# Kernel tuning notes

Measured on AMD Instinct MI355X. Metric: run time of the kernel, lower is better.

The kernel has to match this reference:

```python
import jax, jax.numpy as jnp
import numpy as np

N_NODES = 100000
N_NEIGH = 10
DIM = 256
N_LAYERS = 3


def setup_inputs() -> dict:
    key = jax.random.key(0)
    ks = jax.random.split(key, 8)
    x = jax.random.normal(ks[0], (N_NODES, DIM), dtype=jnp.float32)
    adj = jax.random.randint(ks[1], (N_NODES, N_NEIGH), 0, N_NODES, dtype=jnp.int32)
    # per-layer SAGE weights: Linear(2*D -> D), stored as [2D, D] for x @ W
    scale = 0.05
    W0 = jax.random.normal(ks[2], (2 * DIM, DIM), dtype=jnp.float32) * scale
    W1 = jax.random.normal(ks[3], (2 * DIM, DIM), dtype=jnp.float32) * scale
    W2 = jax.random.normal(ks[4], (2 * DIM, DIM), dtype=jnp.float32) * scale
    b0 = jnp.zeros((DIM,), dtype=jnp.float32)
    b1 = jnp.zeros((DIM,), dtype=jnp.float32)
    b2 = jnp.zeros((DIM,), dtype=jnp.float32)
    return {"x": x, "adj": adj, "W0": W0, "b0": b0, "W1": W1, "b1": b1,
            "W2": W2, "b2": b2}


def reference(x, adj, W0, b0, W1, b1, W2, b2):
    """GraphSAGE: per layer, gather sampled neighbors [N,K,D], mean over K,
    concat with self embedding, linear [2D->D], ReLU on all but last layer."""
    layers = [(W0, b0), (W1, b1), (W2, b2)]
    h = x
    for i, (W, b) in enumerate(layers):
        neigh = jnp.mean(h[adj], axis=1)                 # [N, K, D] -> [N, D]
        h = jnp.concatenate([h, neigh], axis=1) @ W + b  # [N, 2D] @ [2D, D]
        if i < len(layers) - 1:
            h = jax.nn.relu(h)
    return h
```

## Files before the change

kernel.cpp:

```cpp
#include <hip/hip_runtime.h>
#include <stdint.h>

#define NN 100000
#define NK 10
#define D  256
#define D2 512
#define MT 32

typedef short bf16x8 __attribute__((ext_vector_type(8)));
typedef float f32x4  __attribute__((ext_vector_type(4)));

__device__ __forceinline__ uint16_t f2bf(float f) {
  uint32_t u = __float_as_uint(f);
  u += 0x7fffu + ((u >> 16) & 1u);
  return (uint16_t)(u >> 16);
}
__device__ __forceinline__ uint32_t pack2(float a, float b) {
  return (uint32_t)f2bf(a) | ((uint32_t)f2bf(b) << 16);
}

__global__ __launch_bounds__(256) void prep(
    const float* __restrict__ x, uint8_t* __restrict__ q8, float* __restrict__ qs,
    const float* __restrict__ W0, const float* __restrict__ W1,
    const float* __restrict__ W2, uint16_t* __restrict__ Wp0,
    uint16_t* __restrict__ Wp1, uint16_t* __restrict__ Wp2)
{
  const int bid = blockIdx.x;
  if (bid < 192) {
    const float* W;
    uint16_t* Wp;
    if (bid < 64)       { W = W0; Wp = Wp0; }
    else if (bid < 128) { W = W1; Wp = Wp1; }
    else                { W = W2; Wp = Wp2; }
    int idx   = ((bid & 63) << 8) + threadIdx.x;
    int lane  = idx & 63;
    int ntile = (idx >> 6) & 15;
    int kstep = idx >> 10;
    int n  = ntile * 16 + (lane & 15);
    int k0 = kstep * 32 + (lane >> 4) * 8;
    float v[8];
#pragma unroll
    for (int j = 0; j < 8; j++) v[j] = W[(size_t)(k0 + j) * D + n];
    uint4 o;
    o.x = pack2(v[0], v[1]);
    o.y = pack2(v[2], v[3]);
    o.z = pack2(v[4], v[5]);
    o.w = pack2(v[6], v[7]);
    ((uint4*)Wp)[idx] = o;
  } else {
    int node = (bid - 192) * 4 + (threadIdx.x >> 6);
    int lane = threadIdx.x & 63;
    const float4 v = *(const float4*)(x + (size_t)node * D + lane * 4);
    float m = fmaxf(fmaxf(fabsf(v.x), fabsf(v.y)), fmaxf(fabsf(v.z), fabsf(v.w)));
#pragma unroll
    for (int d = 1; d < 64; d <<= 1) m = fmaxf(m, __shfl_xor(m, d, 64));
    float inv = m > 1e-30f ? 127.0f / m : 0.0f;
    int q0 = (int)rintf(v.x * inv), q1 = (int)rintf(v.y * inv);
    int q2 = (int)rintf(v.z * inv), q3 = (int)rintf(v.w * inv);
    uint32_t p = (uint32_t)(q0 & 0xff) | ((uint32_t)(q1 & 0xff) << 8) |
                 ((uint32_t)(q2 & 0xff) << 16) | ((uint32_t)(q3 & 0xff) << 24);
    ((uint32_t*)(q8 + (size_t)node * D))[lane] = p;
    if (lane == 0) qs[node] = m * (1.0f / 127.0f);
  }
}

template <bool SELF_F32, bool QOUT>
__global__ __launch_bounds__(256, 4) void sage_layer(
    const void*     __restrict__ hin_v,
    const uint8_t*  __restrict__ qtab,
    const float*    __restrict__ qsc,
    const int*      __restrict__ adj,
    const uint16_t* __restrict__ Wp,
    const float*    __restrict__ bias,
    void*           __restrict__ hout_v,
    uint8_t*        __restrict__ q8out,
    float*          __restrict__ qsout)
{
  __shared__ uint4 lds4[MT * 64];
  const int t    = threadIdx.x;
  const int m0   = blockIdx.x * MT;
  const int half = t >> 5;
  const int l32  = t & 31;
  const int hb   = half & ~1;
  const int hsel = (half & 1) * 10;

  int av0, av1, av2, av3;
  {
    const int* ap = adj + (size_t)(m0 + hb) * NK;
    int o = (l32 < 20) ? l32 : 0;
    av0 = ap[o];
    av1 = ap[80 + o];
    av2 = ap[160 + o];
    av3 = ap[240 + o];
  }

  uint2 gA[NK], gB[NK];
  float sA[NK], sB[NK];

  auto issue = [&](int av, uint2 (&g)[NK], float (&s)[NK]) {
#pragma unroll
    for (int k = 0; k < NK; k++) {
      int nb = __shfl(av, hsel + k, 32);
      s[k] = qsc[nb];
      g[k] = *(const uint2*)(qtab + (size_t)nb * D + l32 * 8);
    }
  };
  auto consume = [&](const uint2 (&g)[NK], const float (&s)[NK], int i) {
    int r = i * 8 + half;
    float a0=0.f,a1=0.f,a2=0.f,a3=0.f,a4=0.f,a5=0.f,a6=0.f,a7=0.f;
#pragma unroll
    for (int k = 0; k < NK; k++) {
      float sk = s[k];
      uint2 v  = g[k];
      a0 += sk * (float)(int8_t)(v.x);
      a1 += sk * (float)(int8_t)(v.x >> 8);
      a2 += sk * (float)(int8_t)(v.x >> 16);
      a3 += sk * (float)(int8_t)(v.x >> 24);
      a4 += sk * (float)(int8_t)(v.y);
      a5 += sk * (float)(int8_t)(v.y >> 8);
      a6 += sk * (float)(int8_t)(v.y >> 16);
      a7 += sk * (float)(int8_t)(v.y >> 24);
    }
    const float sc = 1.0f / (float)NK;
    uint4 o;
    o.x = pack2(a0 * sc, a1 * sc);
    o.y = pack2(a2 * sc, a3 * sc);
    o.z = pack2(a4 * sc, a5 * sc);
    o.w = pack2(a6 * sc, a7 * sc);
    int c = 32 + l32;
    lds4[r * 64 + (c ^ (r & 15))] = o;
  };

  if constexpr (SELF_F32) {
#pragma unroll
    for (int i = 0; i < 4; i++) {
      int cidx = t + i * 256;
      int r = cidx >> 5, c = cidx & 31;
      const float4* p =
          (const float4*)((const float*)hin_v + (size_t)(m0 + r) * D + c * 8);
      float4 v0 = p[0], v1 = p[1];
      uint4 o;
      o.x = pack2(v0.x, v0.y); o.y = pack2(v0.z, v0.w);
      o.z = pack2(v1.x, v1.y); o.w = pack2(v1.z, v1.w);
      lds4[r * 64 + (c ^ (r & 15))] = o;
    }
    issue(av0, gA, sA);
    issue(av1, gB, sB);
  } else {
    uint4 p1[4];
#pragma unroll
    for (int i = 0; i < 4; i++) {
      int cidx = t + i * 256;
      int r = cidx >> 5, c = cidx & 31;
      p1[i] = *(const uint4*)((const uint16_t*)hin_v + (size_t)(m0 + r) * D + c * 8);
    }
    issue(av0, gA, sA);
    issue(av1, gB, sB);
#pragma unroll
    for (int i = 0; i < 4; i++) {
      int cidx = t + i * 256;
      int r = cidx >> 5, c = cidx & 31;
      lds4[r * 64 + (c ^ (r & 15))] = p1[i];
    }
  }

  consume(gA, sA, 0);
  issue(av2, gA, sA);
  consume(gB, sB, 1);
  issue(av3, gB, sB);
  consume(gA, sA, 2);
  consume(gB, sB, 3);

  __syncthreads();

  const int w    = t >> 6;
  const int l    = t & 63;
  const int quad = l >> 4;
  const int l16  = l & 15;

  f32x4 acc[2][4];
#pragma unroll
  for (int mt = 0; mt < 2; mt++)
#pragma unroll
    for (int nt = 0; nt < 4; nt++)
      acc[mt][nt] = (f32x4){0.f, 0.f, 0.f, 0.f};

  const uint4* wp4 = (const uint4*)Wp;

#pragma unroll 2
  for (int ks = 0; ks < 16; ks++) {
    bf16x8 af[2], bfr[4];
#pragma unroll
    for (int mt = 0; mt < 2; mt++) {
      int row = mt * 16 + l16;
      int c   = ks * 4 + quad;
      af[mt] = *((const bf16x8*)&lds4[row * 64 + (c ^ (row & 15))]);
    }
#pragma unroll
    for (int nt = 0; nt < 4; nt++) {
      bfr[nt] = *((const bf16x8*)&wp4[(ks * 16 + (w * 4 + nt)) * 64 + l]);
    }
#pragma unroll
    for (int mt = 0; mt < 2; mt++)
#pragma unroll
      for (int nt = 0; nt < 4; nt++)
        acc[mt][nt] = __builtin_amdgcn_mfma_f32_16x16x32_bf16(
            af[mt], bfr[nt], acc[mt][nt], 0, 0, 0);
  }

  float lmax[2][4];
#pragma unroll
  for (int mt = 0; mt < 2; mt++)
#pragma unroll
    for (int i = 0; i < 4; i++) lmax[mt][i] = 0.0f;

#pragma unroll
  for (int mt = 0; mt < 2; mt++)
#pragma unroll
    for (int nt = 0; nt < 4; nt++)
#pragma unroll
      for (int i = 0; i < 4; i++) {
        int col = w * 64 + nt * 16 + l16;
        float v = acc[mt][nt][i] + bias[col];
        if (QOUT) v = fmaxf(v, 0.0f);
        acc[mt][nt][i] = v;
        if (QOUT) lmax[mt][i] = fmaxf(lmax[mt][i], v);
      }

  float inv[2][4];
  if (QOUT) {
#pragma unroll
    for (int d = 1; d < 16; d <<= 1)
#pragma unroll
      for (int mt = 0; mt < 2; mt++)
#pragma unroll
        for (int i = 0; i < 4; i++)
          lmax[mt][i] = fmaxf(lmax[mt][i], __shfl_xor(lmax[mt][i], d, 64));
    __syncthreads();
    float* rmax = (float*)lds4;
    if (l16 == 0) {
#pragma unroll
      for (int mt = 0; mt < 2; mt++)
#pragma unroll
        for (int i = 0; i < 4; i++)
          rmax[(mt * 16 + quad * 4 + i) * 4 + w] = lmax[mt][i];
    }
    __syncthreads();
#pragma unroll
    for (int mt = 0; mt < 2; mt++)
#pragma unroll
      for (int i = 0; i < 4; i++) {
        int row = mt * 16 + quad * 4 + i;
        float m = fmaxf(fmaxf(rmax[row * 4 + 0], rmax[row * 4 + 1]),
                        fmaxf(rmax[row * 4 + 2], rmax[row * 4 + 3]));
        inv[mt][i] = m > 1e-30f ? 127.0f / m : 0.0f;
        if (w == 0 && l16 == 0) qsout[m0 + row] = m * (1.0f / 127.0f);
      }
  }

#pragma unroll
  for (int mt = 0; mt < 2; mt++)
#pragma unroll
    for (int i = 0; i < 4; i++) {
      int rr = m0 + mt * 16 + quad * 4 + i;
#pragma unroll
      for (int nt = 0; nt < 4; nt++) {
        int col = w * 64 + nt * 16 + l16;
        float v = acc[mt][nt][i];
        if (QOUT) {
          ((uint16_t*)hout_v)[(size_t)rr * D + col] = f2bf(v);
          int q = (int)rintf(v * inv[mt][i]);
          q8out[(size_t)rr * D + col] = (uint8_t)(q & 0xff);
        } else {
          ((float*)hout_v)[(size_t)rr * D + col] = v;
        }
      }
    }
}

extern "C" void kernel_launch(void* const* d_in, const int* in_sizes, int n_in,
                              void* d_out, int out_size, void* d_ws, size_t ws_size,
                              hipStream_t stream) {
  const float* x   = (const float*)d_in[0];
  const int*   adj = (const int*)d_in[1];
  const float* W0  = (const float*)d_in[2];
  const float* b0  = (const float*)d_in[3];
  const float* W1  = (const float*)d_in[4];
  const float* b1  = (const float*)d_in[5];
  const float* W2  = (const float*)d_in[6];
  const float* b2  = (const float*)d_in[7];
  float* out = (float*)d_out;

  uint8_t*  dob = (uint8_t*)d_out;
  uint16_t* hA  = (uint16_t*)dob;
  uint8_t*  hA8 = dob + 51200000;
  uint8_t*  x8  = dob + 76800000;

  uint16_t* ws  = (uint16_t*)d_ws;
  uint16_t* Wp0 = ws;
  uint16_t* Wp1 = Wp0 + D2 * D;
  uint16_t* Wp2 = Wp1 + D2 * D;
  uint16_t* hB  = Wp2 + D2 * D;
  uint8_t*  hB8 = (uint8_t*)(hB + (size_t)NN * D);
  float*    xs  = (float*)(hB8 + (size_t)NN * D);
  float*    hAs = xs + NN;
  float*    hBs = hAs + NN;

  prep<<<192 + NN / 4, 256, 0, stream>>>(x, x8, xs, W0, W1, W2, Wp0, Wp1, Wp2);

  const int grid = NN / MT;
  sage_layer<true,  true ><<<grid, 256, 0, stream>>>(x,  x8,  xs,  adj, Wp0, b0, hA,  hA8, hAs);
  sage_layer<false, true ><<<grid, 256, 0, stream>>>(hA, hA8, hAs, adj, Wp1, b1, hB,  hB8, hBs);
  sage_layer<false, false><<<grid, 256, 0, stream>>>(hB, hB8, hBs, adj, Wp2, b2, out, nullptr, nullptr);
}
```

Measured before the change: 427.4 us.

## Stream neighbor gathers directly into LDS with per-wave async pipeline

```diff
diff --git a/kernel.cpp b/kernel.cpp
--- a/kernel.cpp
+++ b/kernel.cpp
@@ -17,6 +17,12 @@
 }
 __device__ __forceinline__ uint32_t pack2(float a, float b) {
   return (uint32_t)f2bf(a) | ((uint32_t)f2bf(b) << 16);
+}
+
+__device__ __forceinline__ void gload_lds4(const void* g, void* lds) {
+  __builtin_amdgcn_global_load_lds(
+      (const __attribute__((address_space(1))) uint32_t*)g,
+      (__attribute__((address_space(3))) uint32_t*)lds, 4, 0, 0);
 }
 
 __global__ __launch_bounds__(256) void prep(
@@ -65,7 +71,7 @@
 }
 
 template <bool SELF_F32, bool QOUT>
-__global__ __launch_bounds__(256, 4) void sage_layer(
+__global__ __launch_bounds__(256, 3) void sage_layer(
     const void*     __restrict__ hin_v,
     const uint8_t*  __restrict__ qtab,
     const float*    __restrict__ qsc,
@@ -76,105 +82,103 @@
     uint8_t*        __restrict__ q8out,
     float*          __restrict__ qsout)
 {
-  __shared__ uint4 lds4[MT * 64];
-  const int t    = threadIdx.x;
-  const int m0   = blockIdx.x * MT;
-  const int half = t >> 5;
-  const int l32  = t & 31;
-  const int hb   = half & ~1;
-  const int hsel = (half & 1) * 10;
-
-  int av0, av1, av2, av3;
-  {
-    const int* ap = adj + (size_t)(m0 + hb) * NK;
-    int o = (l32 < 20) ? l32 : 0;
-    av0 = ap[o];
-    av1 = ap[80 + o];
-    av2 = ap[160 + o];
-    av3 = ap[240 + o];
-  }
-
-  uint2 gA[NK], gB[NK];
-  float sA[NK], sB[NK];
-
-  auto issue = [&](int av, uint2 (&g)[NK], float (&s)[NK]) {
-#pragma unroll
-    for (int k = 0; k < NK; k++) {
-      int nb = __shfl(av, hsel + k, 32);
-      s[k] = qsc[nb];
-      g[k] = *(const uint2*)(qtab + (size_t)nb * D + l32 * 8);
-    }
-  };
-  auto consume = [&](const uint2 (&g)[NK], const float (&s)[NK], int i) {
-    int r = i * 8 + half;
-    float a0=0.f,a1=0.f,a2=0.f,a3=0.f,a4=0.f,a5=0.f,a6=0.f,a7=0.f;
-#pragma unroll
-    for (int k = 0; k < NK; k++) {
-      float sk = s[k];
-      uint2 v  = g[k];
-      a0 += sk * (float)(int8_t)(v.x);
-      a1 += sk * (float)(int8_t)(v.x >> 8);
-      a2 += sk * (float)(int8_t)(v.x >> 16);
-      a3 += sk * (float)(int8_t)(v.x >> 24);
-      a4 += sk * (float)(int8_t)(v.y);
-      a5 += sk * (float)(int8_t)(v.y >> 8);
-      a6 += sk * (float)(int8_t)(v.y >> 16);
-      a7 += sk * (float)(int8_t)(v.y >> 24);
-    }
-    const float sc = 1.0f / (float)NK;
-    uint4 o;
-    o.x = pack2(a0 * sc, a1 * sc);
-    o.y = pack2(a2 * sc, a3 * sc);
-    o.z = pack2(a4 * sc, a5 * sc);
-    o.w = pack2(a6 * sc, a7 * sc);
-    int c = 32 + l32;
-    lds4[r * 64 + (c ^ (r & 15))] = o;
-  };
-
-  if constexpr (SELF_F32) {
-#pragma unroll
-    for (int i = 0; i < 4; i++) {
-      int cidx = t + i * 256;
-      int r = cidx >> 5, c = cidx & 31;
+  __shared__ uint4    lds4[MT * 64];
+  __shared__ uint32_t stg[4 * 2 * NK * 64];
+
+  const int t  = threadIdx.x;
+  const int m0 = blockIdx.x * MT;
+  const int w  = t >> 6;
+  const int l  = t & 63;
+
+  const int* ap = adj + (size_t)(m0 + 8 * w) * NK;
+  int av0 = ap[l];
+  int av1 = ap[64 + (l & 15)];
+  __builtin_amdgcn_sched_barrier(0);
+
+  float4 sv[4][2];
+  uint4  sb[4];
+#pragma unroll
+  for (int i = 0; i < 4; i++) {
+    int cidx = t + i * 256;
+    int r = cidx >> 5, c = cidx & 31;
+    if constexpr (SELF_F32) {
       const float4* p =
           (const float4*)((const float*)hin_v + (size_t)(m0 + r) * D + c * 8);
-      float4 v0 = p[0], v1 = p[1];
-      uint4 o;
-      o.x = pack2(v0.x, v0.y); o.y = pack2(v0.z, v0.w);
-      o.z = pack2(v1.x, v1.y); o.w = pack2(v1.z, v1.w);
-      lds4[r * 64 + (c ^ (r & 15))] = o;
-    }
-    issue(av0, gA, sA);
-    issue(av1, gB, sB);
-  } else {
-    uint4 p1[4];
-#pragma unroll
-    for (int i = 0; i < 4; i++) {
-      int cidx = t + i * 256;
-      int r = cidx >> 5, c = cidx & 31;
-      p1[i] = *(const uint4*)((const uint16_t*)hin_v + (size_t)(m0 + r) * D + c * 8);
-    }
-    issue(av0, gA, sA);
-    issue(av1, gB, sB);
-#pragma unroll
-    for (int i = 0; i < 4; i++) {
-      int cidx = t + i * 256;
-      int r = cidx >> 5, c = cidx & 31;
-      lds4[r * 64 + (c ^ (r & 15))] = p1[i];
-    }
-  }
-
-  consume(gA, sA, 0);
-  issue(av2, gA, sA);
-  consume(gB, sB, 1);
-  issue(av3, gB, sB);
-  consume(gA, sA, 2);
-  consume(gB, sB, 3);
+      sv[i][0] = p[0];
+      sv[i][1] = p[1];
+    } else {
+      sb[i] = *(const uint4*)((const uint16_t*)hin_v + (size_t)(m0 + r) * D + c * 8);
+    }
+  }
+  __builtin_amdgcn_sched_barrier(0);
+
+  float sp0 = qsc[av0];
+  float sp1 = qsc[av1];
+  __builtin_amdgcn_sched_barrier(0);
+
+  auto issue_row = [&](int r) {
+#pragma unroll
+    for (int k = 0; k < NK; k++) {
+      const int j = r * NK + k;
+      int nb = (j < 64) ? __shfl(av0, j, 64) : __shfl(av1, j - 64, 64);
+      gload_lds4(qtab + (size_t)nb * D + l * 4,
+                 &stg[(((w << 1) | (r & 1)) * NK + k) * 64]);
+    }
+  };
+
+  issue_row(0);
+  issue_row(1);
+  __builtin_amdgcn_sched_barrier(0);
+
+#pragma unroll
+  for (int i = 0; i < 4; i++) {
+    int cidx = t + i * 256;
+    int r = cidx >> 5, c = cidx & 31;
+    uint4 o;
+    if constexpr (SELF_F32) {
+      o.x = pack2(sv[i][0].x, sv[i][0].y);
+      o.y = pack2(sv[i][0].z, sv[i][0].w);
+      o.z = pack2(sv[i][1].x, sv[i][1].y);
+      o.w = pack2(sv[i][1].z, sv[i][1].w);
+    } else {
+      o = sb[i];
+    }
+    lds4[r * 64 + (c ^ (r & 15))] = o;
+  }
+  __builtin_amdgcn_sched_barrier(0);
+
+  const float scK = 1.0f / (float)NK;
+#pragma unroll
+  for (int r = 0; r < 8; r++) {
+    if (r < 7) asm volatile("s_waitcnt vmcnt(10)" ::: "memory");
+    else       asm volatile("s_waitcnt vmcnt(0)"  ::: "memory");
+    __builtin_amdgcn_sched_barrier(0);
+
+    float c0 = 0.f, c1 = 0.f, c2 = 0.f, c3 = 0.f;
+#pragma unroll
+    for (int k = 0; k < NK; k++) {
+      const int j = r * NK + k;
+      float s = (j < 64) ? __shfl(sp0, j, 64) : __shfl(sp1, j - 64, 64);
+      uint32_t v = stg[(((w << 1) | (r & 1)) * NK + k) * 64 + l];
+      c0 += s * (float)(int8_t)(v);
+      c1 += s * (float)(int8_t)(v >> 8);
+      c2 += s * (float)(int8_t)(v >> 16);
+      c3 += s * (float)(int8_t)(v >> 24);
+    }
+    uint2 o;
+    o.x = pack2(c0 * scK, c1 * scK);
+    o.y = pack2(c2 * scK, c3 * scK);
+    const int r8 = 8 * w + r;
+    const int cc = 32 + (l >> 1);
+    *(uint2*)((uint8_t*)lds4 +
+              ((r8 * 64 + (cc ^ (r8 & 15))) * 16 + (l & 1) * 8)) = o;
+    __builtin_amdgcn_sched_barrier(0);
+    if (r < 6) issue_row(r + 2);
+    __builtin_amdgcn_sched_barrier(0);
+  }
 
   __syncthreads();
 
-  const int w    = t >> 6;
-  const int l    = t & 63;
   const int quad = l >> 4;
   const int l16  = l & 15;
 
```

Measured after the change: 492.2 us. 15.1% more time.

## Hand-schedule gather loads with inline asm and explicit vmcnt waits

Applied to the files above, without the earlier changes.

```diff
diff --git a/kernel.cpp b/kernel.cpp
--- a/kernel.cpp
+++ b/kernel.cpp
@@ -9,6 +9,9 @@
 
 typedef short bf16x8 __attribute__((ext_vector_type(8)));
 typedef float f32x4  __attribute__((ext_vector_type(4)));
+typedef unsigned int vu2a __attribute__((ext_vector_type(2)));
+typedef unsigned int vu4a __attribute__((ext_vector_type(4)));
+typedef float        vf4  __attribute__((ext_vector_type(4)));
 
 __device__ __forceinline__ uint16_t f2bf(float f) {
   uint32_t u = __float_as_uint(f);
@@ -18,6 +21,25 @@
 __device__ __forceinline__ uint32_t pack2(float a, float b) {
   return (uint32_t)f2bf(a) | ((uint32_t)f2bf(b) << 16);
 }
+
+__device__ __forceinline__ void gl_f32(float &d, uint64_t a) {
+  asm volatile("global_load_dword %0, %1, off" : "=v"(d) : "v"(a));
+}
+__device__ __forceinline__ void gl_b64(vu2a &d, uint64_t a) {
+  asm volatile("global_load_dwordx2 %0, %1, off" : "=v"(d) : "v"(a));
+}
+__device__ __forceinline__ void gl_b128(vu4a &d, uint64_t a) {
+  asm volatile("global_load_dwordx4 %0, %1, off" : "=v"(d) : "v"(a));
+}
+#define VMWAIT(N)                                            \
+  do {                                                       \
+    asm volatile("s_waitcnt vmcnt(" #N ")" ::: "memory");    \
+    __builtin_amdgcn_sched_barrier(0);                       \
+  } while (0)
+__device__ __forceinline__ void vsync_i(int &x)    { asm volatile("" : "+v"(x)); }
+__device__ __forceinline__ void vsync_f(float &x)  { asm volatile("" : "+v"(x)); }
+__device__ __forceinline__ void vsync_u2(vu2a &x)  { asm volatile("" : "+v"(x)); }
+__device__ __forceinline__ void vsync_u4(vu4a &x)  { asm volatile("" : "+v"(x)); }
 
 __global__ __launch_bounds__(256) void prep(
     const float* __restrict__ x, uint8_t* __restrict__ q8, float* __restrict__ qs,
@@ -50,7 +72,7 @@
   } else {
     int node = (bid - 192) * 4 + (threadIdx.x >> 6);
     int lane = threadIdx.x & 63;
-    const float4 v = *(const float4*)(x + (size_t)node * D + lane * 4);
+    const vf4 v = *(const vf4*)(x + (size_t)node * D + lane * 4);
     float m = fmaxf(fmaxf(fabsf(v.x), fabsf(v.y)), fmaxf(fabsf(v.z), fabsf(v.w)));
 #pragma unroll
     for (int d = 1; d < 64; d <<= 1) m = fmaxf(m, __shfl_xor(m, d, 64));
@@ -86,32 +108,52 @@
 
   int av0, av1, av2, av3;
   {
-    const int* ap = adj + (size_t)(m0 + hb) * NK;
     int o = (l32 < 20) ? l32 : 0;
-    av0 = ap[o];
-    av1 = ap[80 + o];
-    av2 = ap[160 + o];
-    av3 = ap[240 + o];
-  }
-
-  uint2 gA[NK], gB[NK];
+    uint64_t aa = (uint64_t)(adj + (size_t)(m0 + hb) * NK + o);
+    asm volatile("global_load_dword %0, %1, off"            : "=v"(av0) : "v"(aa));
+    asm volatile("global_load_dword %0, %1, off offset:320" : "=v"(av1) : "v"(aa));
+    asm volatile("global_load_dword %0, %1, off offset:640" : "=v"(av2) : "v"(aa));
+    asm volatile("global_load_dword %0, %1, off offset:960" : "=v"(av3) : "v"(aa));
+  }
+
+  vu4a p1[4];
+  vu4a pf[8];
+#pragma unroll
+  for (int i = 0; i < 4; i++) {
+    int cidx = t + i * 256;
+    int r = cidx >> 5, c = cidx & 31;
+    if constexpr (SELF_F32) {
+      uint64_t a = (uint64_t)((const float*)hin_v + (size_t)(m0 + r) * D + c * 8);
+      gl_b128(pf[2 * i], a);
+      gl_b128(pf[2 * i + 1], a + 16);
+    } else {
+      uint64_t a = (uint64_t)((const uint16_t*)hin_v + (size_t)(m0 + r) * D + c * 8);
+      gl_b128(p1[i], a);
+    }
+  }
+
+  vu2a gA[NK], gB[NK];
   float sA[NK], sB[NK];
 
-  auto issue = [&](int av, uint2 (&g)[NK], float (&s)[NK]) {
+  auto issue = [&](int av, vu2a (&g)[NK], float (&s)[NK]) {
 #pragma unroll
     for (int k = 0; k < NK; k++) {
       int nb = __shfl(av, hsel + k, 32);
-      s[k] = qsc[nb];
-      g[k] = *(const uint2*)(qtab + (size_t)nb * D + l32 * 8);
+      gl_f32(s[k], (uint64_t)(qsc + nb));
+      gl_b64(g[k], (uint64_t)(qtab + (size_t)nb * D + l32 * 8));
     }
   };
-  auto consume = [&](const uint2 (&g)[NK], const float (&s)[NK], int i) {
+  auto sync_buf = [&](vu2a (&g)[NK], float (&s)[NK]) {
+#pragma unroll
+    for (int k = 0; k < NK; k++) { vsync_u2(g[k]); vsync_f(s[k]); }
+  };
+  auto consume = [&](const vu2a (&g)[NK], const float (&s)[NK], int i) {
     int r = i * 8 + half;
     float a0=0.f,a1=0.f,a2=0.f,a3=0.f,a4=0.f,a5=0.f,a6=0.f,a7=0.f;
 #pragma unroll
     for (int k = 0; k < NK; k++) {
       float sk = s[k];
-      uint2 v  = g[k];
+      vu2a v  = g[k];
       a0 += sk * (float)(int8_t)(v.x);
       a1 += sk * (float)(int8_t)(v.x >> 8);
       a2 += sk * (float)(int8_t)(v.x >> 16);
@@ -131,44 +173,59 @@
     lds4[r * 64 + (c ^ (r & 15))] = o;
   };
 
-  if constexpr (SELF_F32) {
+  auto self_to_lds = [&]() {
 #pragma unroll
     for (int i = 0; i < 4; i++) {
       int cidx = t + i * 256;
       int r = cidx >> 5, c = cidx & 31;
-      const float4* p =
-          (const float4*)((const float*)hin_v + (size_t)(m0 + r) * D + c * 8);
-      float4 v0 = p[0], v1 = p[1];
       uint4 o;
-      o.x = pack2(v0.x, v0.y); o.y = pack2(v0.z, v0.w);
-      o.z = pack2(v1.x, v1.y); o.w = pack2(v1.z, v1.w);
+      if constexpr (SELF_F32) {
+        vu4a v0 = pf[2 * i], v1 = pf[2 * i + 1];
+        o.x = pack2(__uint_as_float(v0.x), __uint_as_float(v0.y));
+        o.y = pack2(__uint_as_float(v0.z), __uint_as_float(v0.w));
+        o.z = pack2(__uint_as_float(v1.x), __uint_as_float(v1.y));
+        o.w = pack2(__uint_as_float(v1.z), __uint_as_float(v1.w));
+      } else {
+        vu4a v = p1[i];
+        o.x = v.x; o.y = v.y; o.z = v.z; o.w = v.w;
+      }
       lds4[r * 64 + (c ^ (r & 15))] = o;
     }
+  };
+
+  if constexpr (SELF_F32) {
+    VMWAIT(8);
+    vsync_i(av0); vsync_i(av1); vsync_i(av2); vsync_i(av3);
     issue(av0, gA, sA);
+    VMWAIT(20);
+#pragma unroll
+    for (int i = 0; i < 8; i++) vsync_u4(pf[i]);
+    self_to_lds();
     issue(av1, gB, sB);
+    VMWAIT(20);
   } else {
-    uint4 p1[4];
-#pragma unroll
-    for (int i = 0; i < 4; i++) {
-      int cidx = t + i * 256;
-      int r = cidx >> 5, c = cidx & 31;
-      p1[i] = *(const uint4*)((const uint16_t*)hin_v + (size_t)(m0 + r) * D + c * 8);
-    }
+    VMWAIT(4);
+    vsync_i(av0); vsync_i(av1); vsync_i(av2); vsync_i(av3);
     issue(av0, gA, sA);
+    VMWAIT(20);
+#pragma unroll
+    for (int i = 0; i < 4; i++) vsync_u4(p1[i]);
+    self_to_lds();
     issue(av1, gB, sB);
-#pragma unroll
-    for (int i = 0; i < 4; i++) {
-      int cidx = t + i * 256;
-      int r = cidx >> 5, c = cidx & 31;
-      lds4[r * 64 + (c ^ (r & 15))] = p1[i];
-    }
-  }
-
+    VMWAIT(20);
+  }
+  sync_buf(gA, sA);
   consume(gA, sA, 0);
   issue(av2, gA, sA);
+  VMWAIT(20);
+  sync_buf(gB, sB);
   consume(gB, sB, 1);
   issue(av3, gB, sB);
+  VMWAIT(20);
+  sync_buf(gA, sA);
   consume(gA, sA, 2);
+  VMWAIT(0);
+  sync_buf(gB, sB);
   consume(gB, sB, 3);
 
   __syncthreads();
```

Result: no change. 424.3 us (-0.7%).

## Halve node tile to 16 rows per block and double occupancy target

Applied to the files above, without the earlier changes.

```diff
diff --git a/kernel.cpp b/kernel.cpp
--- a/kernel.cpp
+++ b/kernel.cpp
@@ -5,7 +5,7 @@
 #define NK 10
 #define D  256
 #define D2 512
-#define MT 32
+#define MT 16
 
 typedef short bf16x8 __attribute__((ext_vector_type(8)));
 typedef float f32x4  __attribute__((ext_vector_type(4)));
@@ -65,7 +65,7 @@
 }
 
 template <bool SELF_F32, bool QOUT>
-__global__ __launch_bounds__(256, 4) void sage_layer(
+__global__ __launch_bounds__(256, 8) void sage_layer(
     const void*     __restrict__ hin_v,
     const uint8_t*  __restrict__ qtab,
     const float*    __restrict__ qsc,
@@ -84,14 +84,12 @@
   const int hb   = half & ~1;
   const int hsel = (half & 1) * 10;
 
-  int av0, av1, av2, av3;
+  int av0, av1;
   {
     const int* ap = adj + (size_t)(m0 + hb) * NK;
     int o = (l32 < 20) ? l32 : 0;
     av0 = ap[o];
     av1 = ap[80 + o];
-    av2 = ap[160 + o];
-    av3 = ap[240 + o];
   }
 
   uint2 gA[NK], gB[NK];
@@ -133,7 +131,7 @@
 
   if constexpr (SELF_F32) {
 #pragma unroll
-    for (int i = 0; i < 4; i++) {
+    for (int i = 0; i < 2; i++) {
       int cidx = t + i * 256;
       int r = cidx >> 5, c = cidx & 31;
       const float4* p =
@@ -147,9 +145,9 @@
     issue(av0, gA, sA);
     issue(av1, gB, sB);
   } else {
-    uint4 p1[4];
-#pragma unroll
-    for (int i = 0; i < 4; i++) {
+    uint4 p1[2];
+#pragma unroll
+    for (int i = 0; i < 2; i++) {
       int cidx = t + i * 256;
       int r = cidx >> 5, c = cidx & 31;
       p1[i] = *(const uint4*)((const uint16_t*)hin_v + (size_t)(m0 + r) * D + c * 8);
@@ -157,7 +155,7 @@
     issue(av0, gA, sA);
     issue(av1, gB, sB);
 #pragma unroll
-    for (int i = 0; i < 4; i++) {
+    for (int i = 0; i < 2; i++) {
       int cidx = t + i * 256;
       int r = cidx >> 5, c = cidx & 31;
       lds4[r * 64 + (c ^ (r & 15))] = p1[i];
@@ -165,11 +163,7 @@
   }
 
   consume(gA, sA, 0);
-  issue(av2, gA, sA);
   consume(gB, sB, 1);
-  issue(av3, gB, sB);
-  consume(gA, sA, 2);
-  consume(gB, sB, 3);
 
   __syncthreads();
 
@@ -178,104 +172,86 @@
   const int quad = l >> 4;
   const int l16  = l & 15;
 
-  f32x4 acc[2][4];
-#pragma unroll
-  for (int mt = 0; mt < 2; mt++)
-#pragma unroll
-    for (int nt = 0; nt < 4; nt++)
-      acc[mt][nt] = (f32x4){0.f, 0.f, 0.f, 0.f};
+  f32x4 acc[4];
+#pragma unroll
+  for (int nt = 0; nt < 4; nt++)
+    acc[nt] = (f32x4){0.f, 0.f, 0.f, 0.f};
 
   const uint4* wp4 = (const uint4*)Wp;
 
 #pragma unroll 2
   for (int ks = 0; ks < 16; ks++) {
-    bf16x8 af[2], bfr[4];
-#pragma unroll
-    for (int mt = 0; mt < 2; mt++) {
-      int row = mt * 16 + l16;
+    bf16x8 af, bfr[4];
+    {
+      int row = l16;
       int c   = ks * 4 + quad;
-      af[mt] = *((const bf16x8*)&lds4[row * 64 + (c ^ (row & 15))]);
+      af = *((const bf16x8*)&lds4[row * 64 + (c ^ (row & 15))]);
     }
 #pragma unroll
     for (int nt = 0; nt < 4; nt++) {
       bfr[nt] = *((const bf16x8*)&wp4[(ks * 16 + (w * 4 + nt)) * 64 + l]);
     }
 #pragma unroll
-    for (int mt = 0; mt < 2; mt++)
-#pragma unroll
-      for (int nt = 0; nt < 4; nt++)
-        acc[mt][nt] = __builtin_amdgcn_mfma_f32_16x16x32_bf16(
-            af[mt], bfr[nt], acc[mt][nt], 0, 0, 0);
-  }
-
-  float lmax[2][4];
-#pragma unroll
-  for (int mt = 0; mt < 2; mt++)
-#pragma unroll
-    for (int i = 0; i < 4; i++) lmax[mt][i] = 0.0f;
-
-#pragma unroll
-  for (int mt = 0; mt < 2; mt++)
-#pragma unroll
     for (int nt = 0; nt < 4; nt++)
-#pragma unroll
-      for (int i = 0; i < 4; i++) {
-        int col = w * 64 + nt * 16 + l16;
-        float v = acc[mt][nt][i] + bias[col];
-        if (QOUT) v = fmaxf(v, 0.0f);
-        acc[mt][nt][i] = v;
-        if (QOUT) lmax[mt][i] = fmaxf(lmax[mt][i], v);
-      }
-
-  float inv[2][4];
+      acc[nt] = __builtin_amdgcn_mfma_f32_16x16x32_bf16(af, bfr[nt], acc[nt], 0, 0, 0);
+  }
+
+  float lmax[4];
+#pragma unroll
+  for (int i = 0; i < 4; i++) lmax[i] = 0.0f;
+
+#pragma unroll
+  for (int nt = 0; nt < 4; nt++)
+#pragma unroll
+    for (int i = 0; i < 4; i++) {
+      int col = w * 64 + nt * 16 + l16;
+      float v = acc[nt][i] + bias[col];
+      if (QOUT) v = fmaxf(v, 0.0f);
+      acc[nt][i] = v;
+      if (QOUT) lmax[i] = fmaxf(lmax[i], v);
+    }
+
+  float inv[4];
   if (QOUT) {
 #pragma unroll
     for (int d = 1; d < 16; d <<= 1)
 #pragma unroll
-      for (int mt = 0; mt < 2; mt++)
-#pragma unroll
-        for (int i = 0; i < 4; i++)
-          lmax[mt][i] = fmaxf(lmax[mt][i], __shfl_xor(lmax[mt][i], d, 64));
+      for (int i = 0; i < 4; i++)
+        lmax[i] = fmaxf(lmax[i], __shfl_xor(lmax[i], d, 64));
     __syncthreads();
     float* rmax = (float*)lds4;
     if (l16 == 0) {
 #pragma unroll
-      for (int mt = 0; mt < 2; mt++)
-#pragma unroll
-        for (int i = 0; i < 4; i++)
-          rmax[(mt * 16 + quad * 4 + i) * 4 + w] = lmax[mt][i];
+      for (int i = 0; i < 4; i++)
+        rmax[(quad * 4 + i) * 4 + w] = lmax[i];
     }
     __syncthreads();
 #pragma unroll
-    for (int mt = 0; mt < 2; mt++)
-#pragma unroll
-      for (int i = 0; i < 4; i++) {
-        int row = mt * 16 + quad * 4 + i;
-        float m = fmaxf(fmaxf(rmax[row * 4 + 0], rmax[row * 4 + 1]),
-                        fmaxf(rmax[row * 4 + 2], rmax[row * 4 + 3]));
-        inv[mt][i] = m > 1e-30f ? 127.0f / m : 0.0f;
-        if (w == 0 && l16 == 0) qsout[m0 + row] = m * (1.0f / 127.0f);
+    for (int i = 0; i < 4; i++) {
+      int row = quad * 4 + i;
+      float m = fmaxf(fmaxf(rmax[row * 4 + 0], rmax[row * 4 + 1]),
+                      fmaxf(rmax[row * 4 + 2], rmax[row * 4 + 3]));
+      inv[i] = m > 1e-30f ? 127.0f / m : 0.0f;
+      if (w == 0 && l16 == 0) qsout[m0 + row] = m * (1.0f / 127.0f);
+    }
+  }
+
+#pragma unroll
+  for (int i = 0; i < 4; i++) {
+    int rr = m0 + quad * 4 + i;
+#pragma unroll
+    for (int nt = 0; nt < 4; nt++) {
+      int col = w * 64 + nt * 16 + l16;
+      float v = acc[nt][i];
+      if (QOUT) {
+        ((uint16_t*)hout_v)[(size_t)rr * D + col] = f2bf(v);
+        int q = (int)rintf(v * inv[i]);
+        q8out[(size_t)rr * D + col] = (uint8_t)(q & 0xff);
+      } else {
+        ((float*)hout_v)[(size_t)rr * D + col] = v;
       }
-  }
-
-#pragma unroll
-  for (int mt = 0; mt < 2; mt++)
-#pragma unroll
-    for (int i = 0; i < 4; i++) {
-      int rr = m0 + mt * 16 + quad * 4 + i;
-#pragma unroll
-      for (int nt = 0; nt < 4; nt++) {
-        int col = w * 64 + nt * 16 + l16;
-        float v = acc[mt][nt][i];
-        if (QOUT) {
-          ((uint16_t*)hout_v)[(size_t)rr * D + col] = f2bf(v);
-          int q = (int)rintf(v * inv[mt][i]);
-          q8out[(size_t)rr * D + col] = (uint8_t)(q & 0xff);
-        } else {
-          ((float*)hout_v)[(size_t)rr * D + col] = v;
-        }
-      }
-    }
+    }
+  }
 }
 
 extern "C" void kernel_launch(void* const* d_in, const int* in_sizes, int n_in,
```

New measurement: 481.0 us. 12.5% more time.
